# Kernel tuning notes

Hardware: AMD Instinct MI355X
Metric: run time of the kernel (lower is better)

The kernel has to match this reference:

```python
import jax, jax.numpy as jnp
import numpy as np

N_NODES = 50000
N_EDGES = 800000
IN_FEATS = 256
OUT_FEATS = 32
NUM_HEADS = 8
NUM_ETYPES = 5


def setup_inputs() -> dict:
    key = jax.random.key(0)
    k1, k2, k3, k4, k5, k6 = jax.random.split(key, 6)
    feat = jax.random.normal(k1, (N_NODES, IN_FEATS), dtype=jnp.float32)
    # xavier_normal-ish scale for fc weight [H*D, in]
    fc_w = jax.random.normal(k2, (NUM_HEADS * OUT_FEATS, IN_FEATS), dtype=jnp.float32) * 0.088
    edge_emb = jax.random.normal(k3, (NUM_ETYPES, NUM_HEADS), dtype=jnp.float32)
    e_feat = jax.random.randint(k4, (N_EDGES,), 0, NUM_ETYPES)
    src = jax.random.randint(k5, (N_EDGES,), 0, N_NODES)
    dst = jax.random.randint(k6, (N_EDGES,), 0, N_NODES)
    return {"feat": feat, "fc_w": fc_w, "edge_emb": edge_emb,
            "e_feat": e_feat, "src": src, "dst": dst}


def reference(feat, fc_w, edge_emb, e_feat, src, dst):
    N = feat.shape[0]
    H, D = NUM_HEADS, OUT_FEATS
    # fc: [N, in] @ [in, H*D] -> [N, H, D]
    feat_src = (feat @ fc_w.T).reshape(N, H, D)
    # per-edge, per-head logits from edge-type embedding: [E, H]
    e = edge_emb[e_feat]
    # edge_softmax: softmax over incoming edges of each dst node, per head
    m = jax.ops.segment_max(e, dst, num_segments=N)          # [N, H]
    ex = jnp.exp(e - m[dst])                                  # [E, H]
    denom = jax.ops.segment_sum(ex, dst, num_segments=N)     # [N, H]
    attn = ex / denom[dst]                                    # [E, H]
    # attn_sum: sum of attention weights arriving at each dst (== 1 w/o dropout)
    attn_sum = jax.ops.segment_sum(attn, dst, num_segments=N)  # [N, H]
    # weighted aggregation: sum_e attn_e * feat_src[src_e]
    msg = feat_src[src] * attn[:, :, None]                    # [E, H, D]
    agg = jax.ops.segment_sum(msg, dst, num_segments=N)      # [N, H, D]
    rst = agg / (attn_sum[:, :, None] + 1e-12)
    return rst, attn
```

## Files before the change

### kernel.cpp

```cpp
#include <hip/hip_runtime.h>

typedef unsigned short u16;
typedef unsigned int u32;
typedef __attribute__((ext_vector_type(8))) short bf16x8;
typedef __attribute__((ext_vector_type(4))) float f32x4;
typedef __attribute__((ext_vector_type(2))) float f32x2;

#define NND 50000
#define NE 800000
#define NH 8
#define ND 32
#define NTY 5

__device__ inline u16 f2bf(float x){
  u32 u = __float_as_uint(x);
  return (u16)((u + 0x7FFFu + ((u >> 16) & 1u)) >> 16);
}

__global__ __launch_bounds__(256) void wcvt_k(const float* __restrict__ W,
                                              u16* __restrict__ Wb){
  int i = (blockIdx.x * 256 + threadIdx.x) * 4;
  f32x4 v = __builtin_nontemporal_load((const f32x4*)(W + i));
  ushort4 h = make_ushort4(f2bf(v[0]), f2bf(v[1]), f2bf(v[2]), f2bf(v[3]));
  *(ushort4*)(Wb + i) = h;
}

__global__ __launch_bounds__(512, 4) void gemm_k(const float* __restrict__ A,
                                                 const u16* __restrict__ Wb,
                                                 u16* __restrict__ C, int M){
  __shared__ u16 As[128 * 64];
  __shared__ u16 Ws[256 * 64];
  const int tid  = threadIdx.x;
  const int m0   = blockIdx.x * 128;
  const int lane = tid & 63, wid = tid >> 6;
  const int wm = (wid >> 2) * 64, wn = (wid & 3) * 64;
  const int ml = lane & 15, quad = lane >> 4;

  f32x4 acc[4][4] = {};

  const int ra = tid >> 2, ca0 = (tid & 3) * 2;
  int rag = m0 + ra; if (rag >= M) rag = M - 1;
  const float* aRow = A + (size_t)rag * 256;
  const int rw = tid >> 1, hw = tid & 1;
  const u16* wRow = Wb + (size_t)rw * 256;

  for (int k0 = 0; k0 < 256; k0 += 64){
    #pragma unroll
    for (int q = 0; q < 2; q++){
      int ch = ca0 + q;
      f32x4 v0 = __builtin_nontemporal_load((const f32x4*)(aRow + k0 + ch * 8));
      f32x4 v1 = __builtin_nontemporal_load((const f32x4*)(aRow + k0 + ch * 8 + 4));
      ushort4 h0 = make_ushort4(f2bf(v0[0]), f2bf(v0[1]), f2bf(v0[2]), f2bf(v0[3]));
      ushort4 h1 = make_ushort4(f2bf(v1[0]), f2bf(v1[1]), f2bf(v1[2]), f2bf(v1[3]));
      u16* p = As + ra * 64 + ((ch ^ (ra & 7)) * 8);
      *(ushort4*)p = h0;
      *(ushort4*)(p + 4) = h1;
    }
    #pragma unroll
    for (int q = 0; q < 4; q++){
      int ch = hw * 4 + q;
      uint4 wv = *(const uint4*)(wRow + k0 + ch * 8);
      *(uint4*)(Ws + rw * 64 + ((ch ^ (rw & 7)) * 8)) = wv;
    }
    __syncthreads();
    #pragma unroll
    for (int kk = 0; kk < 64; kk += 32){
      bf16x8 af[4], wf[4];
      const int cA = (kk >> 3) + quad;
      #pragma unroll
      for (int t = 0; t < 4; t++){
        int r = wm + t * 16 + ml;
        af[t] = *(const bf16x8*)(As + r * 64 + ((cA ^ (r & 7)) * 8));
      }
      #pragma unroll
      for (int t = 0; t < 4; t++){
        int n = wn + t * 16 + ml;
        wf[t] = *(const bf16x8*)(Ws + n * 64 + ((cA ^ (n & 7)) * 8));
      }
      #pragma unroll
      for (int i = 0; i < 4; i++)
        #pragma unroll
        for (int j = 0; j < 4; j++)
          acc[i][j] = __builtin_amdgcn_mfma_f32_16x16x32_bf16(af[i], wf[j], acc[i][j], 0, 0, 0);
    }
    __syncthreads();
  }
  const size_t qoff = (size_t)(wn >> 6) * NND * 64;
  #pragma unroll
  for (int i = 0; i < 4; i++){
    #pragma unroll
    for (int rr = 0; rr < 4; rr++){
      int row = m0 + wm + i * 16 + quad * 4 + rr;
      if (row < M){
        u16* crow = C + qoff + (size_t)row * 64;
        #pragma unroll
        for (int j = 0; j < 4; j++)
          __builtin_nontemporal_store(f2bf(acc[i][j][rr]), crow + j * 16 + ml);
      }
    }
  }
}

__global__ __launch_bounds__(256) void count_k(const int* __restrict__ dst,
                                               int* __restrict__ deg,
                                               int* __restrict__ epos){
  int e = blockIdx.x * 256 + threadIdx.x;
  if (e < NE) epos[e] = atomicAdd(&deg[dst[e]], 1);
}

__global__ __launch_bounds__(256) void scan1_k(const int* __restrict__ deg,
                                               int* __restrict__ offs,
                                               int* __restrict__ bsum){
  __shared__ int lds[256];
  int b = blockIdx.x, tid = threadIdx.x;
  int base = b * 1024 + tid * 4;
  int d[4]; int tsum = 0;
  #pragma unroll
  for (int j = 0; j < 4; j++){
    int node = base + j;
    int v = (node < NND) ? deg[node] : 0;
    d[j] = tsum; tsum += v;
  }
  lds[tid] = tsum; __syncthreads();
  for (int off = 1; off < 256; off <<= 1){
    int v = (tid >= off) ? lds[tid - off] : 0;
    __syncthreads();
    lds[tid] += v;
    __syncthreads();
  }
  int excl = lds[tid] - tsum;
  #pragma unroll
  for (int j = 0; j < 4; j++)
    if (base + j < NND) offs[base + j] = excl + d[j];
  if (tid == 255) bsum[b] = lds[tid];
}

__global__ __launch_bounds__(64) void scan2_k(const int* __restrict__ bsum,
                                              int* __restrict__ bbase, int nb){
  __shared__ int l[64];
  int tid = threadIdx.x;
  int v = (tid < nb) ? bsum[tid] : 0;
  l[tid] = v; __syncthreads();
  for (int off = 1; off < 64; off <<= 1){
    int u = (tid >= off) ? l[tid - off] : 0;
    __syncthreads();
    l[tid] += u;
    __syncthreads();
  }
  bbase[tid] = l[tid] - v;
}

__global__ __launch_bounds__(256) void scatter_k(const int* __restrict__ dst,
                                                 const int* __restrict__ src,
                                                 const int* __restrict__ ef,
                                                 const int* __restrict__ epos,
                                                 const int* __restrict__ offs,
                                                 const int* __restrict__ bbase,
                                                 int* __restrict__ csr){
  int e = blockIdx.x * 256 + threadIdx.x;
  if (e >= NE) return;
  int d = dst[e];
  int pos = offs[d] + bbase[d >> 10] + epos[e];
  csr[pos] = (src[e] << 7) | ef[e];
}

__global__ __launch_bounds__(256) void attn_k(const int* __restrict__ dst,
                                              const int* __restrict__ ef,
                                              const float* __restrict__ rdq,
                                              const float* __restrict__ emb,
                                              float* __restrict__ attn){
  __shared__ float wl[40];
  int tid = threadIdx.x;
  if (tid < 40){
    int t = tid >> 3, h = tid & 7;
    float m = emb[h];
    for (int tt = 1; tt < NTY; ++tt) m = fmaxf(m, emb[tt * 8 + h]);
    wl[tid] = expf(emb[t * 8 + h] - m);
  }
  __syncthreads();
  int e = blockIdx.x * 256 + tid;
  if (e >= NE) return;
  int d = dst[e], t = ef[e];
  const float* wr = wl + t * 8;
  f32x4 o0, o1;
  #pragma unroll
  for (int q = 0; q < 4; q++){
    float2 rv = *(const float2*)(rdq + ((size_t)q * NND + d) * 2);
    float a = wr[2 * q] * rv.x, b = wr[2 * q + 1] * rv.y;
    if (q < 2){ o0[2 * q] = a; o0[2 * q + 1] = b; }
    else      { o1[2 * (q - 2)] = a; o1[2 * (q - 2) + 1] = b; }
  }
  __builtin_nontemporal_store(o0, (f32x4*)(attn + (size_t)e * 8));
  __builtin_nontemporal_store(o1, (f32x4*)(attn + (size_t)e * 8 + 4));
}

__device__ inline void acc8(uint4 v, float wt, f32x2* a){
  f32x2 w2; w2.x = wt; w2.y = wt;
  f32x2 t0; t0.x = __uint_as_float(v.x << 16); t0.y = __uint_as_float(v.x & 0xFFFF0000u);
  f32x2 t1; t1.x = __uint_as_float(v.y << 16); t1.y = __uint_as_float(v.y & 0xFFFF0000u);
  f32x2 t2; t2.x = __uint_as_float(v.z << 16); t2.y = __uint_as_float(v.z & 0xFFFF0000u);
  f32x2 t3; t3.x = __uint_as_float(v.w << 16); t3.y = __uint_as_float(v.w & 0xFFFF0000u);
  a[0] += w2 * t0; a[1] += w2 * t1; a[2] += w2 * t2; a[3] += w2 * t3;
}

#define NBLK ((NND + 31) / 32)
#define NBLKP (((NBLK + 7) / 8) * 8)

__global__ __launch_bounds__(256) void agg_k(const u16* __restrict__ fsrc,
                                             const int* __restrict__ csr,
                                             const int* __restrict__ offs,
                                             const int* __restrict__ bbase,
                                             const int* __restrict__ deg,
                                             const float* __restrict__ emb,
                                             float* __restrict__ rst,
                                             float* __restrict__ rdq){
  __shared__ float wl[40];
  int tid = threadIdx.x;
  if (tid < 40){
    int t = tid >> 3, h = tid & 7;
    float m = emb[h];
    for (int tt = 1; tt < NTY; ++tt) m = fmaxf(m, emb[tt * 8 + h]);
    wl[tid] = expf(emb[t * 8 + h] - m);
  }
  __syncthreads();
  const int q  = blockIdx.x / NBLKP;
  const int nb = blockIdx.x % NBLKP;
  if (nb >= NBLK) return;
  int node = nb * 32 + (tid >> 3);
  if (node >= NND) return;
  const int sl = tid & 7;
  const int h  = 2 * q + (sl >> 2);
  const u16* qbase = fsrc + (size_t)q * (NND * 64) + sl * 8;
  int s = offs[node] + bbase[node >> 10];
  int e = s + deg[node];
  f32x2 a[4]; a[0] = 0.f; a[1] = 0.f; a[2] = 0.f; a[3] = 0.f;
  float ss = 0.f;
  int i = s;
  for (; i + 3 < e; i += 4){
    int p0 = csr[i], p1 = csr[i+1], p2 = csr[i+2], p3 = csr[i+3];
    uint4 v0 = *(const uint4*)(qbase + ((size_t)(p0 >> 7) << 6));
    uint4 v1 = *(const uint4*)(qbase + ((size_t)(p1 >> 7) << 6));
    uint4 v2 = *(const uint4*)(qbase + ((size_t)(p2 >> 7) << 6));
    uint4 v3 = *(const uint4*)(qbase + ((size_t)(p3 >> 7) << 6));
    float w0 = wl[(p0 & 7) * 8 + h];
    float w1 = wl[(p1 & 7) * 8 + h];
    float w2 = wl[(p2 & 7) * 8 + h];
    float w3 = wl[(p3 & 7) * 8 + h];
    acc8(v0, w0, a); acc8(v1, w1, a); acc8(v2, w2, a); acc8(v3, w3, a);
    ss += (w0 + w1) + (w2 + w3);
  }
  for (; i < e; i++){
    int p0 = csr[i];
    uint4 v0 = *(const uint4*)(qbase + ((size_t)(p0 >> 7) << 6));
    float w0 = wl[(p0 & 7) * 8 + h];
    acc8(v0, w0, a);
    ss += w0;
  }
  float inv = 1.0f / (ss + 1e-12f);
  f32x4 o0, o1;
  o0[0] = a[0].x*inv; o0[1] = a[0].y*inv; o0[2] = a[1].x*inv; o0[3] = a[1].y*inv;
  o1[0] = a[2].x*inv; o1[1] = a[2].y*inv; o1[2] = a[3].x*inv; o1[3] = a[3].y*inv;
  float* orow = rst + (size_t)node * 256 + q * 64 + sl * 8;
  __builtin_nontemporal_store(o0, (f32x4*)orow);
  __builtin_nontemporal_store(o1, (f32x4*)(orow + 4));
  if ((sl & 3) == 0)
    __builtin_nontemporal_store(inv, rdq + ((size_t)q * NND + node) * 2 + (sl >> 2));
}

extern "C" void kernel_launch(void* const* d_in, const int* in_sizes, int n_in,
                              void* d_out, int out_size, void* d_ws, size_t ws_size,
                              hipStream_t stream) {
  const float* feat = (const float*)d_in[0];
  const float* fcw  = (const float*)d_in[1];
  const float* emb  = (const float*)d_in[2];
  const int*   ef   = (const int*)d_in[3];
  const int*   src  = (const int*)d_in[4];
  const int*   dst  = (const int*)d_in[5];

  float* rst  = (float*)d_out;
  float* attn = (float*)d_out + (size_t)NND * NH * ND;

  char* ws = (char*)d_ws;
  size_t o = 0;
  u16* fsrc    = (u16*)(ws + o);   o += (size_t)NND * 256 * 2;
  int* csr     = (int*)(ws + o);   o += (size_t)NE * 4;
  int* epos    = (int*)(ws + o);   o += (size_t)NE * 4;
  int* offs    = (int*)(ws + o);   o += 200064;
  int* deg     = (int*)(ws + o);   o += 200064;
  float* rdq   = (float*)(ws + o); o += (size_t)NND * NH * 4;
  u16* wb      = (u16*)(ws + o);   o += (size_t)256 * 256 * 2;
  int* bsum    = (int*)(ws + o);   o += 256;
  int* bbase   = (int*)(ws + o);   o += 256;

  hipMemsetAsync(deg, 0, (size_t)NND * 4, stream);

  wcvt_k<<<64, 256, 0, stream>>>(fcw, wb);
  gemm_k<<<391, 512, 0, stream>>>(feat, wb, fsrc, NND);
  count_k<<<(NE + 255) / 256, 256, 0, stream>>>(dst, deg, epos);
  scan1_k<<<(NND + 1023) / 1024, 256, 0, stream>>>(deg, offs, bsum);
  scan2_k<<<1, 64, 0, stream>>>(bsum, bbase, (NND + 1023) / 1024);
  scatter_k<<<(NE + 255) / 256, 256, 0, stream>>>(dst, src, ef, epos, offs, bbase, csr);
  agg_k<<<4 * NBLKP, 256, 0, stream>>>(fsrc, csr, offs, bbase, deg, emb, rst, rdq);
  attn_k<<<(NE + 255) / 256, 256, 0, stream>>>(dst, ef, rdq, emb, attn);
}
```

Measured before the change: 270.8 us.

## Store projected features per head and aggregate one head per block

The GEMM output is rewritten from four 64-wide head-pair planes into eight 32-wide per-head planes. The aggregation kernel now assigns one head per block and four lanes per node, interleaving head on the low bits of blockIdx, so each gathered row is 64 bytes. The per-node reciprocal buffer becomes per-head, and CSR index loads become nontemporal. The intent is a smaller per-head working set that fits better in cache for random gathers, at the cost of reading the CSR list eight times instead of four and running twice as many blocks.

```diff
diff --git a/kernel.cpp b/kernel.cpp
--- a/kernel.cpp
+++ b/kernel.cpp
@@ -85,17 +85,19 @@
     }
     __syncthreads();
   }
-  const size_t qoff = (size_t)(wn >> 6) * NND * 64;
+  const int hb = wn >> 5;
   #pragma unroll
   for (int i = 0; i < 4; i++){
     #pragma unroll
     for (int rr = 0; rr < 4; rr++){
       int row = m0 + wm + i * 16 + quad * 4 + rr;
       if (row < M){
-        u16* crow = C + qoff + (size_t)row * 64;
-        #pragma unroll
-        for (int j = 0; j < 4; j++)
-          __builtin_nontemporal_store(f2bf(acc[i][j][rr]), crow + j * 16 + ml);
+        u16* r0 = C + ((size_t)hb       * NND + row) * 32 + ml;
+        u16* r1 = C + ((size_t)(hb + 1) * NND + row) * 32 + ml;
+        __builtin_nontemporal_store(f2bf(acc[i][0][rr]), r0);
+        __builtin_nontemporal_store(f2bf(acc[i][1][rr]), r0 + 16);
+        __builtin_nontemporal_store(f2bf(acc[i][2][rr]), r1);
+        __builtin_nontemporal_store(f2bf(acc[i][3][rr]), r1 + 16);
       }
     }
   }
@@ -166,7 +168,7 @@
 
 __global__ __launch_bounds__(256) void attn_k(const int* __restrict__ dst,
                                               const int* __restrict__ ef,
-                                              const float* __restrict__ rdq,
+                                              const float* __restrict__ rdh,
                                               const float* __restrict__ emb,
                                               float* __restrict__ attn){
   __shared__ float wl[40];
@@ -184,11 +186,10 @@
   const float* wr = wl + t * 8;
   f32x4 o0, o1;
   #pragma unroll
-  for (int q = 0; q < 4; q++){
-    float2 rv = *(const float2*)(rdq + ((size_t)q * NND + d) * 2);
-    float a = wr[2 * q] * rv.x, b = wr[2 * q + 1] * rv.y;
-    if (q < 2){ o0[2 * q] = a; o0[2 * q + 1] = b; }
-    else      { o1[2 * (q - 2)] = a; o1[2 * (q - 2) + 1] = b; }
+  for (int h = 0; h < 8; h++){
+    float r = rdh[(size_t)h * NND + d];
+    float v = wr[h] * r;
+    if (h < 4) o0[h] = v; else o1[h - 4] = v;
   }
   __builtin_nontemporal_store(o0, (f32x4*)(attn + (size_t)e * 8));
   __builtin_nontemporal_store(o1, (f32x4*)(attn + (size_t)e * 8 + 4));
@@ -203,8 +204,7 @@
   a[0] += w2 * t0; a[1] += w2 * t1; a[2] += w2 * t2; a[3] += w2 * t3;
 }
 
-#define NBLK ((NND + 31) / 32)
-#define NBLKP (((NBLK + 7) / 8) * 8)
+#define NBAGG ((NND + 63) / 64)
 
 __global__ __launch_bounds__(256) void agg_k(const u16* __restrict__ fsrc,
                                              const int* __restrict__ csr,
@@ -213,46 +213,47 @@
                                              const int* __restrict__ deg,
                                              const float* __restrict__ emb,
                                              float* __restrict__ rst,
-                                             float* __restrict__ rdq){
-  __shared__ float wl[40];
-  int tid = threadIdx.x;
-  if (tid < 40){
-    int t = tid >> 3, h = tid & 7;
+                                             float* __restrict__ rdh){
+  __shared__ float wl5[8];
+  const int tid = threadIdx.x;
+  const int h  = blockIdx.x & 7;
+  const int nb = blockIdx.x >> 3;
+  if (tid < NTY){
     float m = emb[h];
     for (int tt = 1; tt < NTY; ++tt) m = fmaxf(m, emb[tt * 8 + h]);
-    wl[tid] = expf(emb[t * 8 + h] - m);
+    wl5[tid] = expf(emb[tid * 8 + h] - m);
   }
   __syncthreads();
-  const int q  = blockIdx.x / NBLKP;
-  const int nb = blockIdx.x % NBLKP;
-  if (nb >= NBLK) return;
-  int node = nb * 32 + (tid >> 3);
+  int node = nb * 64 + (tid >> 2);
   if (node >= NND) return;
-  const int sl = tid & 7;
-  const int h  = 2 * q + (sl >> 2);
-  const u16* qbase = fsrc + (size_t)q * (NND * 64) + sl * 8;
+  const int sl = tid & 2 ? (tid & 3) : (tid & 3);
+  const int sl4 = tid & 3;
+  const u16* hbase = fsrc + (size_t)h * (NND * 32) + sl4 * 8;
   int s = offs[node] + bbase[node >> 10];
   int e = s + deg[node];
   f32x2 a[4]; a[0] = 0.f; a[1] = 0.f; a[2] = 0.f; a[3] = 0.f;
   float ss = 0.f;
   int i = s;
   for (; i + 3 < e; i += 4){
-    int p0 = csr[i], p1 = csr[i+1], p2 = csr[i+2], p3 = csr[i+3];
-    uint4 v0 = *(const uint4*)(qbase + ((size_t)(p0 >> 7) << 6));
-    uint4 v1 = *(const uint4*)(qbase + ((size_t)(p1 >> 7) << 6));
-    uint4 v2 = *(const uint4*)(qbase + ((size_t)(p2 >> 7) << 6));
-    uint4 v3 = *(const uint4*)(qbase + ((size_t)(p3 >> 7) << 6));
-    float w0 = wl[(p0 & 7) * 8 + h];
-    float w1 = wl[(p1 & 7) * 8 + h];
-    float w2 = wl[(p2 & 7) * 8 + h];
-    float w3 = wl[(p3 & 7) * 8 + h];
+    int p0 = __builtin_nontemporal_load(csr + i);
+    int p1 = __builtin_nontemporal_load(csr + i + 1);
+    int p2 = __builtin_nontemporal_load(csr + i + 2);
+    int p3 = __builtin_nontemporal_load(csr + i + 3);
+    uint4 v0 = *(const uint4*)(hbase + ((size_t)(p0 >> 7) << 5));
+    uint4 v1 = *(const uint4*)(hbase + ((size_t)(p1 >> 7) << 5));
+    uint4 v2 = *(const uint4*)(hbase + ((size_t)(p2 >> 7) << 5));
+    uint4 v3 = *(const uint4*)(hbase + ((size_t)(p3 >> 7) << 5));
+    float w0 = wl5[p0 & 7];
+    float w1 = wl5[p1 & 7];
+    float w2 = wl5[p2 & 7];
+    float w3 = wl5[p3 & 7];
     acc8(v0, w0, a); acc8(v1, w1, a); acc8(v2, w2, a); acc8(v3, w3, a);
     ss += (w0 + w1) + (w2 + w3);
   }
   for (; i < e; i++){
-    int p0 = csr[i];
-    uint4 v0 = *(const uint4*)(qbase + ((size_t)(p0 >> 7) << 6));
-    float w0 = wl[(p0 & 7) * 8 + h];
+    int p0 = __builtin_nontemporal_load(csr + i);
+    uint4 v0 = *(const uint4*)(hbase + ((size_t)(p0 >> 7) << 5));
+    float w0 = wl5[p0 & 7];
     acc8(v0, w0, a);
     ss += w0;
   }
@@ -260,11 +261,11 @@
   f32x4 o0, o1;
   o0[0] = a[0].x*inv; o0[1] = a[0].y*inv; o0[2] = a[1].x*inv; o0[3] = a[1].y*inv;
   o1[0] = a[2].x*inv; o1[1] = a[2].y*inv; o1[2] = a[3].x*inv; o1[3] = a[3].y*inv;
-  float* orow = rst + (size_t)node * 256 + q * 64 + sl * 8;
+  float* orow = rst + (size_t)node * 256 + h * 32 + sl4 * 8;
   __builtin_nontemporal_store(o0, (f32x4*)orow);
   __builtin_nontemporal_store(o1, (f32x4*)(orow + 4));
-  if ((sl & 3) == 0)
-    __builtin_nontemporal_store(inv, rdq + ((size_t)q * NND + node) * 2 + (sl >> 2));
+  if (sl4 == 0)
+    __builtin_nontemporal_store(inv, rdh + (size_t)h * NND + node);
 }
 
 extern "C" void kernel_launch(void* const* d_in, const int* in_sizes, int n_in,
@@ -287,7 +288,7 @@
   int* epos    = (int*)(ws + o);   o += (size_t)NE * 4;
   int* offs    = (int*)(ws + o);   o += 200064;
   int* deg     = (int*)(ws + o);   o += 200064;
-  float* rdq   = (float*)(ws + o); o += (size_t)NND * NH * 4;
+  float* rdh   = (float*)(ws + o); o += (size_t)NND * NH * 4;
   u16* wb      = (u16*)(ws + o);   o += (size_t)256 * 256 * 2;
   int* bsum    = (int*)(ws + o);   o += 256;
   int* bbase   = (int*)(ws + o);   o += 256;
@@ -300,6 +301,6 @@
   scan1_k<<<(NND + 1023) / 1024, 256, 0, stream>>>(deg, offs, bsum);
   scan2_k<<<1, 64, 0, stream>>>(bsum, bbase, (NND + 1023) / 1024);
   scatter_k<<<(NE + 255) / 256, 256, 0, stream>>>(dst, src, ef, epos, offs, bbase, csr);
-  agg_k<<<4 * NBLKP, 256, 0, stream>>>(fsrc, csr, offs, bbase, deg, emb, rst, rdq);
-  attn_k<<<(NE + 255) / 256, 256, 0, stream>>>(dst, ef, rdq, emb, attn);
-}
+  agg_k<<<8 * NBAGG, 256, 0, stream>>>(fsrc, csr, offs, bbase, deg, emb, rst, rdh);
+  attn_k<<<(NE + 255) / 256, 256, 0, stream>>>(dst, ef, rdh, emb, attn);
+}
```

After: 320.3 us. 18.3% more time.

## Bucket CSR edges by source-range within each destination and interleave aggregation blocks

Applied to the files above, without the earlier changes.

The CSR build now counts and scans four buckets per destination, keyed by source index high bits, so each node's incoming edges are ordered by source region. The aggregation grid is re-indexed so consecutive blocks cover adjacent node chunks across all four head-quarters. Together these aim to improve L2 locality of the gathered bf16 feature rows. In exchange the degree, offset and scan arrays grow fourfold, and the second scan stage widens to 256 threads.

```diff
diff --git a/kernel.cpp b/kernel.cpp
--- a/kernel.cpp
+++ b/kernel.cpp
@@ -11,6 +11,8 @@
 #define NH 8
 #define ND 32
 #define NTY 5
+#define NV (NND * 4)
+#define SQSH 14
 
 __device__ inline u16 f2bf(float x){
   u32 u = __float_as_uint(x);
@@ -102,14 +104,18 @@
 }
 
 __global__ __launch_bounds__(256) void count_k(const int* __restrict__ dst,
-                                               int* __restrict__ deg,
+                                               const int* __restrict__ src,
+                                               int* __restrict__ deg4,
                                                int* __restrict__ epos){
   int e = blockIdx.x * 256 + threadIdx.x;
-  if (e < NE) epos[e] = atomicAdd(&deg[dst[e]], 1);
-}
-
-__global__ __launch_bounds__(256) void scan1_k(const int* __restrict__ deg,
-                                               int* __restrict__ offs,
+  if (e < NE){
+    int v = dst[e] * 4 + (src[e] >> SQSH);
+    epos[e] = atomicAdd(&deg4[v], 1);
+  }
+}
+
+__global__ __launch_bounds__(256) void scan1_k(const int* __restrict__ deg4,
+                                               int* __restrict__ offs4,
                                                int* __restrict__ bsum){
   __shared__ int lds[256];
   int b = blockIdx.x, tid = threadIdx.x;
@@ -117,8 +123,7 @@
   int d[4]; int tsum = 0;
   #pragma unroll
   for (int j = 0; j < 4; j++){
-    int node = base + j;
-    int v = (node < NND) ? deg[node] : 0;
+    int v = (base + j < NV) ? deg4[base + j] : 0;
     d[j] = tsum; tsum += v;
   }
   lds[tid] = tsum; __syncthreads();
@@ -131,17 +136,17 @@
   int excl = lds[tid] - tsum;
   #pragma unroll
   for (int j = 0; j < 4; j++)
-    if (base + j < NND) offs[base + j] = excl + d[j];
+    if (base + j < NV) offs4[base + j] = excl + d[j];
   if (tid == 255) bsum[b] = lds[tid];
 }
 
-__global__ __launch_bounds__(64) void scan2_k(const int* __restrict__ bsum,
-                                              int* __restrict__ bbase, int nb){
-  __shared__ int l[64];
+__global__ __launch_bounds__(256) void scan2_k(const int* __restrict__ bsum,
+                                               int* __restrict__ bbase, int nb){
+  __shared__ int l[256];
   int tid = threadIdx.x;
   int v = (tid < nb) ? bsum[tid] : 0;
   l[tid] = v; __syncthreads();
-  for (int off = 1; off < 64; off <<= 1){
+  for (int off = 1; off < 256; off <<= 1){
     int u = (tid >= off) ? l[tid - off] : 0;
     __syncthreads();
     l[tid] += u;
@@ -154,14 +159,15 @@
                                                  const int* __restrict__ src,
                                                  const int* __restrict__ ef,
                                                  const int* __restrict__ epos,
-                                                 const int* __restrict__ offs,
-                                                 const int* __restrict__ bbase,
+                                                 const int* __restrict__ offs4,
+                                                 const int* __restrict__ bbase4,
                                                  int* __restrict__ csr){
   int e = blockIdx.x * 256 + threadIdx.x;
   if (e >= NE) return;
-  int d = dst[e];
-  int pos = offs[d] + bbase[d >> 10] + epos[e];
-  csr[pos] = (src[e] << 7) | ef[e];
+  int sv = src[e];
+  int v = dst[e] * 4 + (sv >> SQSH);
+  int pos = offs4[v] + bbase4[v >> 10] + epos[e];
+  csr[pos] = (sv << 7) | ef[e];
 }
 
 __global__ __launch_bounds__(256) void attn_k(const int* __restrict__ dst,
@@ -204,13 +210,13 @@
 }
 
 #define NBLK ((NND + 31) / 32)
-#define NBLKP (((NBLK + 7) / 8) * 8)
+#define NBH  ((NBLK + 1) / 2)
 
 __global__ __launch_bounds__(256) void agg_k(const u16* __restrict__ fsrc,
                                              const int* __restrict__ csr,
-                                             const int* __restrict__ offs,
-                                             const int* __restrict__ bbase,
-                                             const int* __restrict__ deg,
+                                             const int* __restrict__ offs4,
+                                             const int* __restrict__ bbase4,
+                                             const int* __restrict__ deg4,
                                              const float* __restrict__ emb,
                                              float* __restrict__ rst,
                                              float* __restrict__ rdq){
@@ -223,37 +229,39 @@
     wl[tid] = expf(emb[t * 8 + h] - m);
   }
   __syncthreads();
-  const int q  = blockIdx.x / NBLKP;
-  const int nb = blockIdx.x % NBLKP;
-  if (nb >= NBLK) return;
+  const int c  = blockIdx.x & 7;
+  const int q  = c >> 1;
+  const int nb = (blockIdx.x >> 3) * 2 + (c & 1);
   int node = nb * 32 + (tid >> 3);
   if (node >= NND) return;
   const int sl = tid & 7;
   const int h  = 2 * q + (sl >> 2);
   const u16* qbase = fsrc + (size_t)q * (NND * 64) + sl * 8;
-  int s = offs[node] + bbase[node >> 10];
-  int e = s + deg[node];
+  const int v0 = node * 4;
+  int s = offs4[v0] + bbase4[v0 >> 10];
+  int4 dg = *(const int4*)(deg4 + v0);
+  int e = s + dg.x + dg.y + dg.z + dg.w;
   f32x2 a[4]; a[0] = 0.f; a[1] = 0.f; a[2] = 0.f; a[3] = 0.f;
   float ss = 0.f;
   int i = s;
   for (; i + 3 < e; i += 4){
     int p0 = csr[i], p1 = csr[i+1], p2 = csr[i+2], p3 = csr[i+3];
-    uint4 v0 = *(const uint4*)(qbase + ((size_t)(p0 >> 7) << 6));
-    uint4 v1 = *(const uint4*)(qbase + ((size_t)(p1 >> 7) << 6));
-    uint4 v2 = *(const uint4*)(qbase + ((size_t)(p2 >> 7) << 6));
-    uint4 v3 = *(const uint4*)(qbase + ((size_t)(p3 >> 7) << 6));
+    uint4 v0g = *(const uint4*)(qbase + ((size_t)(p0 >> 7) << 6));
+    uint4 v1g = *(const uint4*)(qbase + ((size_t)(p1 >> 7) << 6));
+    uint4 v2g = *(const uint4*)(qbase + ((size_t)(p2 >> 7) << 6));
+    uint4 v3g = *(const uint4*)(qbase + ((size_t)(p3 >> 7) << 6));
     float w0 = wl[(p0 & 7) * 8 + h];
     float w1 = wl[(p1 & 7) * 8 + h];
     float w2 = wl[(p2 & 7) * 8 + h];
     float w3 = wl[(p3 & 7) * 8 + h];
-    acc8(v0, w0, a); acc8(v1, w1, a); acc8(v2, w2, a); acc8(v3, w3, a);
+    acc8(v0g, w0, a); acc8(v1g, w1, a); acc8(v2g, w2, a); acc8(v3g, w3, a);
     ss += (w0 + w1) + (w2 + w3);
   }
   for (; i < e; i++){
     int p0 = csr[i];
-    uint4 v0 = *(const uint4*)(qbase + ((size_t)(p0 >> 7) << 6));
+    uint4 v0g = *(const uint4*)(qbase + ((size_t)(p0 >> 7) << 6));
     float w0 = wl[(p0 & 7) * 8 + h];
-    acc8(v0, w0, a);
+    acc8(v0g, w0, a);
     ss += w0;
   }
   float inv = 1.0f / (ss + 1e-12f);
@@ -285,21 +293,21 @@
   u16* fsrc    = (u16*)(ws + o);   o += (size_t)NND * 256 * 2;
   int* csr     = (int*)(ws + o);   o += (size_t)NE * 4;
   int* epos    = (int*)(ws + o);   o += (size_t)NE * 4;
-  int* offs    = (int*)(ws + o);   o += 200064;
-  int* deg     = (int*)(ws + o);   o += 200064;
+  int* offs4   = (int*)(ws + o);   o += (size_t)NV * 4 + 256;
+  int* deg4    = (int*)(ws + o);   o += (size_t)NV * 4 + 256;
   float* rdq   = (float*)(ws + o); o += (size_t)NND * NH * 4;
   u16* wb      = (u16*)(ws + o);   o += (size_t)256 * 256 * 2;
-  int* bsum    = (int*)(ws + o);   o += 256;
-  int* bbase   = (int*)(ws + o);   o += 256;
-
-  hipMemsetAsync(deg, 0, (size_t)NND * 4, stream);
+  int* bsum    = (int*)(ws + o);   o += 1024;
+  int* bbase4  = (int*)(ws + o);   o += 1024;
+
+  hipMemsetAsync(deg4, 0, (size_t)NV * 4, stream);
 
   wcvt_k<<<64, 256, 0, stream>>>(fcw, wb);
   gemm_k<<<391, 512, 0, stream>>>(feat, wb, fsrc, NND);
-  count_k<<<(NE + 255) / 256, 256, 0, stream>>>(dst, deg, epos);
-  scan1_k<<<(NND + 1023) / 1024, 256, 0, stream>>>(deg, offs, bsum);
-  scan2_k<<<1, 64, 0, stream>>>(bsum, bbase, (NND + 1023) / 1024);
-  scatter_k<<<(NE + 255) / 256, 256, 0, stream>>>(dst, src, ef, epos, offs, bbase, csr);
-  agg_k<<<4 * NBLKP, 256, 0, stream>>>(fsrc, csr, offs, bbase, deg, emb, rst, rdq);
+  count_k<<<(NE + 255) / 256, 256, 0, stream>>>(dst, src, deg4, epos);
+  scan1_k<<<(NV + 1023) / 1024, 256, 0, stream>>>(deg4, offs4, bsum);
+  scan2_k<<<1, 256, 0, stream>>>(bsum, bbase4, (NV + 1023) / 1024);
+  scatter_k<<<(NE + 255) / 256, 256, 0, stream>>>(dst, src, ef, epos, offs4, bbase4, csr);
+  agg_k<<<8 * NBH, 256, 0, stream>>>(fsrc, csr, offs4, bbase4, deg4, emb, rst, rdq);
   attn_k<<<(NE + 255) / 256, 256, 0, stream>>>(dst, ef, rdq, emb, attn);
 }
```

Result: faster. 263.2 us (-2.8%).
